# Kernel tuning notes

Measured on AMD Instinct MI355X. Metric: run time of the kernel, lower is better.

## Reference

```python
import math
import jax, jax.numpy as jnp
import numpy as np

B, S, D, H = 4, 2048, 512, 8
DH = D // H
NUM_BUCKETS = 32
MAX_DISTANCE = 128


def _relative_position_bucket(rel_pos, num_buckets=NUM_BUCKETS, max_distance=MAX_DISTANCE):
    # bidirectional T5 bucketing (faithful to the torch staticmethod)
    num_buckets = num_buckets // 2
    rel_buckets = (rel_pos > 0).astype(jnp.int32) * num_buckets
    rel_pos = jnp.abs(rel_pos)
    max_exact = num_buckets // 2
    is_small = rel_pos < max_exact
    # clamp log arg to >=1 element to avoid -inf cast (masked out by is_small anyway)
    rp_f = jnp.maximum(rel_pos, 1).astype(jnp.float32)
    large = max_exact + (
        jnp.log(rp_f / max_exact) / math.log(max_distance / max_exact) * (num_buckets - max_exact)
    ).astype(jnp.int32)
    large = jnp.minimum(large, num_buckets - 1)
    return rel_buckets + jnp.where(is_small, rel_pos, large)


def setup_inputs() -> dict:
    rng = jax.random.key(0)
    ks = jax.random.split(rng, 12)
    s = 0.02
    return {
        'key':   jax.random.normal(ks[0], (B, S, D), jnp.float32),
        'value': jax.random.normal(ks[1], (B, S, D), jnp.float32),
        'query': jax.random.normal(ks[2], (B, S, D), jnp.float32),
        'Wq': jax.random.normal(ks[3], (D, D), jnp.float32) * s,
        'bq': jnp.zeros((D,), jnp.float32),
        'Wk': jax.random.normal(ks[4], (D, D), jnp.float32) * s,
        'bk': jnp.zeros((D,), jnp.float32),
        'Wv': jax.random.normal(ks[5], (D, D), jnp.float32) * s,
        'bv': jnp.zeros((D,), jnp.float32),
        'Wo': jax.random.normal(ks[6], (D, D), jnp.float32) * s,
        'bo': jnp.zeros((D,), jnp.float32),
        'rel_bias': jax.random.normal(ks[7], (NUM_BUCKETS, H), jnp.float32) * s,
        'mask': jax.random.bernoulli(ks[8], 0.5, (B, S, S)),
    }


def reference(key, value, query, Wq, bq, Wk, bk, Wv, bv, Wo, bo, rel_bias, mask):
    def shape(x):  # [B,S,D] -> [B,H,S,DH]
        return x.reshape(B, -1, H, DH).transpose(0, 2, 1, 3)

    q = shape(query @ Wq + bq) / math.sqrt(DH)
    k = shape(key @ Wk + bk)
    v = shape(value @ Wv + bv)

    scores = jnp.einsum('bhqd,bhkd->bhqk', q, k)  # [B,H,S,S]

    # T5 relative position bias
    rel_pos = jnp.arange(S)[None, :] - jnp.arange(S)[:, None]  # [S,S] memory - query
    buckets = _relative_position_bucket(rel_pos)
    pos_bias = rel_bias[buckets]                     # [S,S,H]
    scores = scores + pos_bias.transpose(2, 0, 1)[None]  # [1,H,S,S]

    scores = jnp.where(mask[:, None, :, :], jnp.float32(-1e18), scores)
    attn = jax.nn.softmax(scores, axis=-1)  # dropout p=0 -> identity

    ctx = jnp.einsum('bhqk,bhkd->bhqd', attn, v)
    ctx = ctx.transpose(0, 2, 1, 3).reshape(B, -1, D)
    return ctx @ Wo + bo
```

## Files before the change

### kernel.cpp

```cpp
#include <hip/hip_runtime.h>
#include <hip/hip_bf16.h>
#include <math.h>

#define BB 4
#define SS 2048
#define DD 512
#define HH 8
#define DHH 64
#define KPAD 72
#define GPAD 72
#define LOG2E 1.44269504088896340736f

typedef __attribute__((ext_vector_type(8))) short short8;
typedef __attribute__((ext_vector_type(4))) float f32x4;
typedef __attribute__((ext_vector_type(16))) float f32x16;
typedef __attribute__((ext_vector_type(4))) unsigned short ushort4v;
typedef unsigned short ushort;
typedef unsigned char uchar;
typedef unsigned int u32;
typedef unsigned long long u64;

static __device__ __forceinline__ ushort f2b(float x) {
    __hip_bfloat16 h = __float2bfloat16(x);
    return *reinterpret_cast<ushort*>(&h);
}

__global__ __launch_bounds__(256) void pack_mask_kernel(const void* __restrict__ mask,
                                                        u64* __restrict__ mwords) {
    __shared__ int sflag;
    const int tid = threadIdx.x;
    if (tid == 0) sflag = 0;
    __syncthreads();
    u32 probe = ((const u32*)mask)[tid];
    if (__any(probe > 1u) && (tid & 63) == 0) sflag = 1;
    __syncthreads();
    const bool bytemode = sflag != 0;

    int idx = blockIdx.x * 256 + tid;
    int w = idx & 31;
    int row = idx >> 5;
    u64 bits = 0ull;
    if (bytemode) {
        const uint4* p4 = (const uint4*)((const uchar*)mask + (size_t)row * SS + w * 64);
#pragma unroll
        for (int i = 0; i < 4; ++i) {
            uint4 v = p4[i];
            unsigned int a[4] = {v.x, v.y, v.z, v.w};
#pragma unroll
            for (int j = 0; j < 4; ++j)
#pragma unroll
                for (int byte = 0; byte < 4; ++byte)
                    if ((a[j] >> (byte * 8)) & 0xffu) bits |= 1ull << (i * 16 + j * 4 + byte);
        }
    } else {
        const int4* p4 = (const int4*)((const int*)mask + (size_t)row * SS + w * 64);
#pragma unroll
        for (int i = 0; i < 16; ++i) {
            int4 v = p4[i];
            if (v.x) bits |= 1ull << (i * 4 + 0);
            if (v.y) bits |= 1ull << (i * 4 + 1);
            if (v.z) bits |= 1ull << (i * 4 + 2);
            if (v.w) bits |= 1ull << (i * 4 + 3);
        }
    }
    mwords[idx] = bits;
}

__device__ __forceinline__ int t5_bucket(int rel) {
    int rb = (rel > 0) ? 16 : 0;
    int ap = rel < 0 ? -rel : rel;
    if (ap < 8) return rb + ap;
    float t = logf((float)ap * 0.125f) / 2.77258872985839844f * 8.0f;
    int large = 8 + (int)t;
    if (large > 15) large = 15;
    return rb + large;
}

__global__ __launch_bounds__(256) void bias_table_kernel(const float* __restrict__ rel_bias,
                                                         float* __restrict__ tbl) {
    int i = blockIdx.x * 256 + threadIdx.x;
    int h = i >> 12;
    int d = (i & 4095) - 2047;
    tbl[i] = LOG2E * rel_bias[t5_bucket(d) * HH + h];
}

__global__ __launch_bounds__(256) void wtrans_kernel(const float* __restrict__ W0, const float* __restrict__ W1,
                                                     const float* __restrict__ W2, const float* __restrict__ W3,
                                                     ushort* __restrict__ T0, ushort* __restrict__ T1,
                                                     ushort* __restrict__ T2, ushort* __restrict__ T3) {
    __shared__ float tile[64][65];
    const float* W = blockIdx.z == 0 ? W0 : blockIdx.z == 1 ? W1 : blockIdx.z == 2 ? W2 : W3;
    ushort*     T = blockIdx.z == 0 ? T0 : blockIdx.z == 1 ? T1 : blockIdx.z == 2 ? T2 : T3;
    const int n0 = blockIdx.x * 64, k0 = blockIdx.y * 64;
    const int tr = threadIdx.x >> 4, tc = threadIdx.x & 15;
#pragma unroll
    for (int i = 0; i < 4; ++i) {
        int r = i * 16 + tr;
        float4 v = *(const float4*)&W[(size_t)(k0 + r) * 512 + n0 + tc * 4];
        tile[r][tc * 4 + 0] = v.x; tile[r][tc * 4 + 1] = v.y;
        tile[r][tc * 4 + 2] = v.z; tile[r][tc * 4 + 3] = v.w;
    }
    __syncthreads();
#pragma unroll
    for (int i = 0; i < 4; ++i) {
        int rn = i * 16 + tr;
        ushort4v o;
#pragma unroll
        for (int j = 0; j < 4; ++j) o[j] = f2b(tile[tc * 4 + j][rn]);
        *(ushort4v*)&T[(size_t)(n0 + rn) * 512 + k0 + tc * 4] = o;
    }
}

__global__ __launch_bounds__(256) void qkv_gemm(const float* __restrict__ Xq, const float* __restrict__ Xk,
                                                const float* __restrict__ Xv,
                                                const ushort* __restrict__ Wqt, const ushort* __restrict__ Wkt,
                                                const ushort* __restrict__ Wvt,
                                                const float* __restrict__ bqp, const float* __restrict__ bkp,
                                                const float* __restrict__ bvp,
                                                ushort* __restrict__ Yq, ushort* __restrict__ Yk,
                                                ushort* __restrict__ Yv) {
    __shared__ ushort Als[64 * GPAD];
    __shared__ ushort Bls[128 * GPAD];
    const int z = blockIdx.z;
    const float* A    = z == 0 ? Xq : z == 1 ? Xk : Xv;
    const ushort* Bt  = z == 0 ? Wqt : z == 1 ? Wkt : Wvt;
    const float* bias = z == 0 ? bqp : z == 1 ? bkp : bvp;
    const float scale = z == 0 ? 0.125f * LOG2E : 1.0f;

    const int tid = threadIdx.x;
    const int lane = tid & 63;
    const int wid = tid >> 6;
    const int lq = lane & 15, lg = lane >> 4;
    const int wr = wid >> 1, wc = wid & 1;
    const int bm = blockIdx.x * 64;
    const int bn = blockIdx.y * 128;

    f32x4 acc[2][4];
#pragma unroll
    for (int m = 0; m < 2; ++m)
#pragma unroll
        for (int n = 0; n < 4; ++n) acc[m][n] = (f32x4){0.f, 0.f, 0.f, 0.f};

    for (int k0 = 0; k0 < 512; k0 += 64) {
        __syncthreads();
#pragma unroll
        for (int i = 0; i < 2; ++i) {
            int c = tid + i * 256;
            int r = c >> 3, kc = (c & 7) * 8;
            float4 u = *(const float4*)(A + (size_t)(bm + r) * 512 + k0 + kc);
            float4 v = *(const float4*)(A + (size_t)(bm + r) * 512 + k0 + kc + 4);
            short8 av;
            av[0] = (short)f2b(u.x); av[1] = (short)f2b(u.y); av[2] = (short)f2b(u.z); av[3] = (short)f2b(u.w);
            av[4] = (short)f2b(v.x); av[5] = (short)f2b(v.y); av[6] = (short)f2b(v.z); av[7] = (short)f2b(v.w);
            *(short8*)&Als[r * GPAD + kc] = av;
        }
#pragma unroll
        for (int i = 0; i < 4; ++i) {
            int c = tid + i * 256;
            int r = c >> 3, kc = (c & 7) * 8;
            *(short8*)&Bls[r * GPAD + kc] = *(const short8*)(Bt + (size_t)(bn + r) * 512 + k0 + kc);
        }
        __syncthreads();
#pragma unroll
        for (int kk = 0; kk < 2; ++kk) {
            short8 af[2], bf[4];
#pragma unroll
            for (int m = 0; m < 2; ++m)
                af[m] = *(short8*)&Als[(wr * 32 + m * 16 + lq) * GPAD + kk * 32 + lg * 8];
#pragma unroll
            for (int n = 0; n < 4; ++n)
                bf[n] = *(short8*)&Bls[(wc * 64 + n * 16 + lq) * GPAD + kk * 32 + lg * 8];
#pragma unroll
            for (int m = 0; m < 2; ++m)
#pragma unroll
                for (int n = 0; n < 4; ++n)
                    acc[m][n] = __builtin_amdgcn_mfma_f32_16x16x32_bf16(af[m], bf[n], acc[m][n], 0, 0, 0);
        }
    }

    float bv[4];
#pragma unroll
    for (int n = 0; n < 4; ++n) bv[n] = bias[bn + wc * 64 + n * 16 + lq];

    if (z == 2) {
        const int blk = bm >> 11;
        const int s0 = (bm & 2047) + wr * 32 + lg * 4;
#pragma unroll
        for (int m = 0; m < 2; ++m)
#pragma unroll
            for (int n = 0; n < 4; ++n) {
                int col = bn + wc * 64 + n * 16 + lq;
                ushort4v o;
#pragma unroll
                for (int r = 0; r < 4; ++r) o[r] = f2b(acc[m][n][r] + bv[n]);
                *(ushort4v*)&Yv[((size_t)(blk * 512 + col)) * SS + s0 + m * 16] = o;
            }
    } else {
        ushort* Y = z ? Yk : Yq;
#pragma unroll
        for (int m = 0; m < 2; ++m)
#pragma unroll
            for (int r = 0; r < 4; ++r) {
                int row = bm + wr * 32 + m * 16 + lg * 4 + r;
#pragma unroll
                for (int n = 0; n < 4; ++n) {
                    int col = bn + wc * 64 + n * 16 + lq;
                    Y[(size_t)row * 512 + col] = f2b((acc[m][n][r] + bv[n]) * scale);
                }
            }
    }
}

__global__ __launch_bounds__(256) void out_gemm(const ushort* __restrict__ A,
                                                const ushort* __restrict__ Bt,
                                                const float* __restrict__ bias,
                                                float* __restrict__ Y) {
    __shared__ ushort Als[64 * GPAD];
    __shared__ ushort Bls[128 * GPAD];
    const int tid = threadIdx.x;
    const int lane = tid & 63;
    const int wid = tid >> 6;
    const int lq = lane & 15, lg = lane >> 4;
    const int wr = wid >> 1, wc = wid & 1;
    const int bm = blockIdx.x * 64;
    const int bn = blockIdx.y * 128;

    f32x4 acc[2][4];
#pragma unroll
    for (int m = 0; m < 2; ++m)
#pragma unroll
        for (int n = 0; n < 4; ++n) acc[m][n] = (f32x4){0.f, 0.f, 0.f, 0.f};

    for (int k0 = 0; k0 < 512; k0 += 64) {
        __syncthreads();
#pragma unroll
        for (int i = 0; i < 2; ++i) {
            int c = tid + i * 256;
            int r = c >> 3, kc = (c & 7) * 8;
            *(short8*)&Als[r * GPAD + kc] = *(const short8*)(A + (size_t)(bm + r) * 512 + k0 + kc);
        }
#pragma unroll
        for (int i = 0; i < 4; ++i) {
            int c = tid + i * 256;
            int r = c >> 3, kc = (c & 7) * 8;
            *(short8*)&Bls[r * GPAD + kc] = *(const short8*)(Bt + (size_t)(bn + r) * 512 + k0 + kc);
        }
        __syncthreads();
#pragma unroll
        for (int kk = 0; kk < 2; ++kk) {
            short8 af[2], bf[4];
#pragma unroll
            for (int m = 0; m < 2; ++m)
                af[m] = *(short8*)&Als[(wr * 32 + m * 16 + lq) * GPAD + kk * 32 + lg * 8];
#pragma unroll
            for (int n = 0; n < 4; ++n)
                bf[n] = *(short8*)&Bls[(wc * 64 + n * 16 + lq) * GPAD + kk * 32 + lg * 8];
#pragma unroll
            for (int m = 0; m < 2; ++m)
#pragma unroll
                for (int n = 0; n < 4; ++n)
                    acc[m][n] = __builtin_amdgcn_mfma_f32_16x16x32_bf16(af[m], bf[n], acc[m][n], 0, 0, 0);
        }
    }

    float bv[4];
#pragma unroll
    for (int n = 0; n < 4; ++n) bv[n] = bias[bn + wc * 64 + n * 16 + lq];
#pragma unroll
    for (int m = 0; m < 2; ++m)
#pragma unroll
        for (int r = 0; r < 4; ++r) {
            int row = bm + wr * 32 + m * 16 + lg * 4 + r;
#pragma unroll
            for (int n = 0; n < 4; ++n) {
                int col = bn + wc * 64 + n * 16 + lq;
                Y[(size_t)row * 512 + col] = acc[m][n][r] + bv[n];
            }
        }
}

__global__ __launch_bounds__(512, 4) void attn_kernel(const ushort* __restrict__ Qg, const ushort* __restrict__ Kg,
                                                      const ushort* __restrict__ vT, const u64* __restrict__ mwords,
                                                      const float* __restrict__ btbl, ushort* __restrict__ ctxb) {
    __shared__ ushort KV[4][64 * KPAD];
    __shared__ ushort QT[128 * KPAD];
    float* tbl = (float*)QT;

    const int bid = blockIdx.x;
    const int wk = ((bid & 7) << 6) | (bid >> 3);
    const int qb = wk & 15;
    const int h  = (wk >> 4) & 7;
    const int b  = wk >> 7;
    const int q0 = qb * 128;

    const int tid  = threadIdx.x;
    const int wid  = tid >> 6;
    const int lane = tid & 63;
    const int lq32 = lane & 31;
    const int hi   = lane >> 5;
    const int seg  = wid >> 2;
    const int qw   = wid & 3;

    const u64* mrow = mwords + (size_t)b * SS * 32;
    const int qg = q0 + qw * 32 + lq32;

    {
        const int r = tid >> 2;
        const int c = (tid & 3) * 16;
        const size_t g = ((size_t)(b * SS + q0 + r)) * DD + h * DHH + c;
        *(short8*)&QT[r * KPAD + c]     = *(const short8*)(Qg + g);
        *(short8*)&QT[r * KPAD + c + 8] = *(const short8*)(Qg + g + 8);
    }
    __syncthreads();

    short8 qf[4];
#pragma unroll
    for (int dch = 0; dch < 4; ++dch)
        qf[dch] = *(short8*)&QT[(qw * 32 + lq32) * KPAD + dch * 16 + hi * 8];
    __syncthreads();

    {
        const float4* src = (const float4*)(btbl + (size_t)h * 4096);
        float4* dst = (float4*)tbl;
        dst[tid]       = src[tid];
        dst[tid + 512] = src[tid + 512];
    }

    f32x16 acc0, acc1, accl;
#pragma unroll
    for (int i = 0; i < 16; ++i) { acc0[i] = 0.f; acc1[i] = 0.f; accl[i] = 0.f; }

    short8 ones;
#pragma unroll
    for (int i = 0; i < 8; ++i) ones[i] = (short)0x3F80;

    const int stile = tid >> 7;
    const int sidx = tid & 127;
    const int srow = sidx >> 1;
    const int scol = (sidx & 1) * 32;
    const size_t kbaseK = ((size_t)(b * SS + (stile & 1) * 1024 + srow)) * DD + h * DHH + scol;
    const size_t kbaseV = ((size_t)(b * DD + h * DHH + srow)) * SS + (stile & 1) * 1024 + scol;

    short8 stg[4];
    {
        const ushort* sp = (stile < 2) ? (Kg + kbaseK) : (vT + kbaseV);
#pragma unroll
        for (int j = 0; j < 4; ++j) stg[j] = *(const short8*)(sp + j * 8);
    }

    const float* tbp_base = tbl + (2047 + hi * 4 - qg);

    for (int t = 0; t < 16; ++t) {
        __syncthreads();
        {
            ushort* dst = &KV[stile][srow * KPAD + scol];
#pragma unroll
            for (int j = 0; j < 4; ++j) *(short8*)(dst + j * 8) = stg[j];
        }
        __syncthreads();
        if (t < 15) {
            const ushort* sp = (stile < 2) ? (Kg + kbaseK + (size_t)(t + 1) * 64 * DD)
                                           : (vT + kbaseV + (t + 1) * 64);
#pragma unroll
            for (int j = 0; j < 4; ++j) stg[j] = *(const short8*)(sp + j * 8);
        }

        const ushort* Ks = KV[seg];
        const ushort* Vt = KV[2 + seg];
        const int ktw = seg * 16 + t;
        const u64 wv = mrow[(size_t)qg * 32 + ktw];

        const float* tbp = tbp_base + ktw * 64;
        f32x16 st0, st1;
#pragma unroll
        for (int r = 0; r < 16; ++r) {
            const int br = (r & 3) + 8 * (r >> 2);
            st0[r] = tbp[br];
            st1[r] = tbp[32 + br];
        }
#pragma unroll
        for (int dch = 0; dch < 4; ++dch) {
            short8 kf0 = *(short8*)&Ks[lq32 * KPAD + dch * 16 + hi * 8];
            short8 kf1 = *(short8*)&Ks[(32 + lq32) * KPAD + dch * 16 + hi * 8];
            st0 = __builtin_amdgcn_mfma_f32_32x32x16_bf16(kf0, qf[dch], st0, 0, 0, 0);
            st1 = __builtin_amdgcn_mfma_f32_32x32x16_bf16(kf1, qf[dch], st1, 0, 0, 0);
        }

        const u32 mi0 = ~(((u32)wv) >> (hi * 4));
        const u32 mi1 = ~(((u32)(wv >> 32)) >> (hi * 4));
        float p0[16], p1[16];
#pragma unroll
        for (int r = 0; r < 16; ++r) {
            const int br = (r & 3) + 8 * (r >> 2);
            float e0 = __builtin_amdgcn_exp2f(st0[r]);
            float e1 = __builtin_amdgcn_exp2f(st1[r]);
            u32 k0 = (u32)(((int)(mi0 << (31 - br))) >> 31);
            u32 k1 = (u32)(((int)(mi1 << (31 - br))) >> 31);
            p0[r] = __uint_as_float(__float_as_uint(e0) & k0);
            p1[r] = __uint_as_float(__float_as_uint(e1) & k1);
        }

        u32 W[16];
#pragma unroll
        for (int w = 0; w < 8; ++w) {
            asm("v_cvt_pk_bf16_f32 %0, %1, %2" : "=v"(W[w])     : "v"(p0[2 * w]), "v"(p0[2 * w + 1]));
            asm("v_cvt_pk_bf16_f32 %0, %1, %2" : "=v"(W[8 + w]) : "v"(p1[2 * w]), "v"(p1[2 * w + 1]));
        }
        short8 pf[4];
#pragma unroll
        for (int g = 0; g < 4; ++g) {
            u32 A = W[g * 4 + 0], Bw = W[g * 4 + 1], C = W[g * 4 + 2], D = W[g * 4 + 3];
            asm("v_permlane32_swap_b32 %0, %1" : "+v"(A), "+v"(C));
            asm("v_permlane32_swap_b32 %0, %1" : "+v"(Bw), "+v"(D));
            u32 fr[4] = {A, Bw, C, D};
            pf[g] = *(short8*)fr;
        }

#pragma unroll
        for (int g = 0; g < 4; ++g) {
            short8 vf0 = *(short8*)&Vt[lq32 * KPAD + g * 16 + hi * 8];
            short8 vf1 = *(short8*)&Vt[(32 + lq32) * KPAD + g * 16 + hi * 8];
            acc0 = __builtin_amdgcn_mfma_f32_32x32x16_bf16(vf0, pf[g], acc0, 0, 0, 0);
            acc1 = __builtin_amdgcn_mfma_f32_32x32x16_bf16(vf1, pf[g], acc1, 0, 0, 0);
            accl = __builtin_amdgcn_mfma_f32_32x32x16_bf16(ones, pf[g], accl, 0, 0, 0);
        }
    }

    float l_run = accl[0];

    __syncthreads();
    float* cmb = (float*)KV;
    float* cl  = cmb + 128 * 65;
    const int q = qw * 32 + lq32;
    if (seg == 1) {
#pragma unroll
        for (int r = 0; r < 16; ++r) {
            const int dr = (r & 3) + 8 * (r >> 2) + 4 * hi;
            cmb[q * 65 + dr]      = acc0[r];
            cmb[q * 65 + 32 + dr] = acc1[r];
        }
        if (hi == 0) cl[q] = l_run;
    }
    __syncthreads();
    if (seg == 0) {
#pragma unroll
        for (int r = 0; r < 16; ++r) {
            const int dr = (r & 3) + 8 * (r >> 2) + 4 * hi;
            acc0[r] += cmb[q * 65 + dr];
            acc1[r] += cmb[q * 65 + 32 + dr];
        }
        l_run += cl[q];
        const float linv = 1.0f / l_run;
        ushort* T = QT;
#pragma unroll
        for (int r = 0; r < 16; ++r) {
            const int dr = (r & 3) + 8 * (r >> 2) + 4 * hi;
            T[q * KPAD + dr]      = f2b(acc0[r] * linv);
            T[q * KPAD + 32 + dr] = f2b(acc1[r] * linv);
        }
        const int r2 = qw * 32 + (lane >> 1);
        const int c0 = (lane & 1) * 32;
        const size_t g = ((size_t)(b * SS + q0 + r2)) * DD + h * DHH + c0;
#pragma unroll
        for (int j = 0; j < 4; ++j)
            *(short8*)(ctxb + g + j * 8) = *(short8*)&QT[r2 * KPAD + c0 + j * 8];
    }
}

extern "C" void kernel_launch(void* const* d_in, const int* in_sizes, int n_in,
                              void* d_out, int out_size, void* d_ws, size_t ws_size,
                              hipStream_t stream) {
    const float* key   = (const float*)d_in[0];
    const float* value = (const float*)d_in[1];
    const float* query = (const float*)d_in[2];
    const float* Wq = (const float*)d_in[3];
    const float* bq = (const float*)d_in[4];
    const float* Wk = (const float*)d_in[5];
    const float* bk = (const float*)d_in[6];
    const float* Wv = (const float*)d_in[7];
    const float* bv = (const float*)d_in[8];
    const float* Wo = (const float*)d_in[9];
    const float* bo = (const float*)d_in[10];
    const float* rel_bias = (const float*)d_in[11];
    const void* mask = d_in[12];
    float* out = (float*)d_out;

    char* ws = (char*)d_ws;
    const size_t MB = 1024 * 1024;
    float* btbl   = (float*)(ws + 4096);
    u64* mwords   = (u64*)(ws + 512 * 1024);
    ushort* wq_t  = (ushort*)(ws + (size_t)(3 * MB));
    ushort* wk_t  = wq_t + 512 * 512;
    ushort* wv_t  = wk_t + 512 * 512;
    ushort* wo_t  = wv_t + 512 * 512;
    ushort* q_bf  = (ushort*)(ws + (size_t)(5 * MB));
    ushort* k_bf  = q_bf + (size_t)8192 * 512;
    ushort* vT    = k_bf + (size_t)8192 * 512;
    ushort* ctx_bf = vT + (size_t)8192 * 512;

    hipLaunchKernelGGL(pack_mask_kernel, dim3(BB * SS * 32 / 256), dim3(256), 0, stream,
                       mask, mwords);
    hipLaunchKernelGGL(bias_table_kernel, dim3(HH * 4096 / 256), dim3(256), 0, stream,
                       rel_bias, btbl);
    hipLaunchKernelGGL(wtrans_kernel, dim3(8, 8, 4), dim3(256), 0, stream,
                       Wq, Wk, Wv, Wo, wq_t, wk_t, wv_t, wo_t);

    hipLaunchKernelGGL(qkv_gemm, dim3(128, 4, 3), dim3(256), 0, stream,
                       query, key, value, wq_t, wk_t, wv_t, bq, bk, bv, q_bf, k_bf, vT);

    hipLaunchKernelGGL(attn_kernel, dim3(512), dim3(512), 0, stream,
                       q_bf, k_bf, vT, mwords, btbl, ctx_bf);

    hipLaunchKernelGGL(out_gemm, dim3(128, 4), dim3(256), 0, stream, ctx_bf, wo_t, bo, out);
}
```

Baseline: 128.8 us.

## Merge prep kernels and register-prefetch GEMMs with larger 128x128 tiles

Fuses the mask packing, bias table and weight transpose kernels into a single prep launch to cut launch overhead. Both projection GEMMs now use 512-thread blocks with 128x128 tiles. They prefetch the next K-slice into registers while MFMAs run on the current LDS tile, so global loads overlap compute. The price is more registers per thread, double the LDS for A, and half as many blocks in the grid, which may lower occupancy.

```diff
diff --git a/kernel.cpp b/kernel.cpp
--- a/kernel.cpp
+++ b/kernel.cpp
@@ -25,47 +25,6 @@
     return *reinterpret_cast<ushort*>(&h);
 }
 
-__global__ __launch_bounds__(256) void pack_mask_kernel(const void* __restrict__ mask,
-                                                        u64* __restrict__ mwords) {
-    __shared__ int sflag;
-    const int tid = threadIdx.x;
-    if (tid == 0) sflag = 0;
-    __syncthreads();
-    u32 probe = ((const u32*)mask)[tid];
-    if (__any(probe > 1u) && (tid & 63) == 0) sflag = 1;
-    __syncthreads();
-    const bool bytemode = sflag != 0;
-
-    int idx = blockIdx.x * 256 + tid;
-    int w = idx & 31;
-    int row = idx >> 5;
-    u64 bits = 0ull;
-    if (bytemode) {
-        const uint4* p4 = (const uint4*)((const uchar*)mask + (size_t)row * SS + w * 64);
-#pragma unroll
-        for (int i = 0; i < 4; ++i) {
-            uint4 v = p4[i];
-            unsigned int a[4] = {v.x, v.y, v.z, v.w};
-#pragma unroll
-            for (int j = 0; j < 4; ++j)
-#pragma unroll
-                for (int byte = 0; byte < 4; ++byte)
-                    if ((a[j] >> (byte * 8)) & 0xffu) bits |= 1ull << (i * 16 + j * 4 + byte);
-        }
-    } else {
-        const int4* p4 = (const int4*)((const int*)mask + (size_t)row * SS + w * 64);
-#pragma unroll
-        for (int i = 0; i < 16; ++i) {
-            int4 v = p4[i];
-            if (v.x) bits |= 1ull << (i * 4 + 0);
-            if (v.y) bits |= 1ull << (i * 4 + 1);
-            if (v.z) bits |= 1ull << (i * 4 + 2);
-            if (v.w) bits |= 1ull << (i * 4 + 3);
-        }
-    }
-    mwords[idx] = bits;
-}
-
 __device__ __forceinline__ int t5_bucket(int rel) {
     int rb = (rel > 0) ? 16 : 0;
     int ap = rel < 0 ? -rel : rel;
@@ -76,42 +35,85 @@
     return rb + large;
 }
 
-__global__ __launch_bounds__(256) void bias_table_kernel(const float* __restrict__ rel_bias,
-                                                         float* __restrict__ tbl) {
-    int i = blockIdx.x * 256 + threadIdx.x;
-    int h = i >> 12;
-    int d = (i & 4095) - 2047;
-    tbl[i] = LOG2E * rel_bias[t5_bucket(d) * HH + h];
-}
-
-__global__ __launch_bounds__(256) void wtrans_kernel(const float* __restrict__ W0, const float* __restrict__ W1,
-                                                     const float* __restrict__ W2, const float* __restrict__ W3,
-                                                     ushort* __restrict__ T0, ushort* __restrict__ T1,
-                                                     ushort* __restrict__ T2, ushort* __restrict__ T3) {
+__global__ __launch_bounds__(256) void prep_kernel(const void* __restrict__ mask, u64* __restrict__ mwords,
+                                                   const float* __restrict__ rel_bias, float* __restrict__ btbl,
+                                                   const float* __restrict__ W0, const float* __restrict__ W1,
+                                                   const float* __restrict__ W2, const float* __restrict__ W3,
+                                                   ushort* __restrict__ T0, ushort* __restrict__ T1,
+                                                   ushort* __restrict__ T2, ushort* __restrict__ T3) {
     __shared__ float tile[64][65];
-    const float* W = blockIdx.z == 0 ? W0 : blockIdx.z == 1 ? W1 : blockIdx.z == 2 ? W2 : W3;
-    ushort*     T = blockIdx.z == 0 ? T0 : blockIdx.z == 1 ? T1 : blockIdx.z == 2 ? T2 : T3;
-    const int n0 = blockIdx.x * 64, k0 = blockIdx.y * 64;
-    const int tr = threadIdx.x >> 4, tc = threadIdx.x & 15;
-#pragma unroll
-    for (int i = 0; i < 4; ++i) {
-        int r = i * 16 + tr;
-        float4 v = *(const float4*)&W[(size_t)(k0 + r) * 512 + n0 + tc * 4];
-        tile[r][tc * 4 + 0] = v.x; tile[r][tc * 4 + 1] = v.y;
-        tile[r][tc * 4 + 2] = v.z; tile[r][tc * 4 + 3] = v.w;
-    }
-    __syncthreads();
-#pragma unroll
-    for (int i = 0; i < 4; ++i) {
-        int rn = i * 16 + tr;
-        ushort4v o;
-#pragma unroll
-        for (int j = 0; j < 4; ++j) o[j] = f2b(tile[tc * 4 + j][rn]);
-        *(ushort4v*)&T[(size_t)(n0 + rn) * 512 + k0 + tc * 4] = o;
-    }
-}
-
-__global__ __launch_bounds__(256) void qkv_gemm(const float* __restrict__ Xq, const float* __restrict__ Xk,
+    __shared__ int sflag;
+    const int bid = blockIdx.x;
+    const int tid = threadIdx.x;
+
+    if (bid < 1024) {
+        if (tid == 0) sflag = 0;
+        __syncthreads();
+        u32 probe = ((const u32*)mask)[tid];
+        if (__any(probe > 1u) && (tid & 63) == 0) sflag = 1;
+        __syncthreads();
+        const bool bytemode = sflag != 0;
+
+        int idx = bid * 256 + tid;
+        int w = idx & 31;
+        int row = idx >> 5;
+        u64 bits = 0ull;
+        if (bytemode) {
+            const uint4* p4 = (const uint4*)((const uchar*)mask + (size_t)row * SS + w * 64);
+#pragma unroll
+            for (int i = 0; i < 4; ++i) {
+                uint4 v = p4[i];
+                unsigned int a[4] = {v.x, v.y, v.z, v.w};
+#pragma unroll
+                for (int j = 0; j < 4; ++j)
+#pragma unroll
+                    for (int byte = 0; byte < 4; ++byte)
+                        if ((a[j] >> (byte * 8)) & 0xffu) bits |= 1ull << (i * 16 + j * 4 + byte);
+            }
+        } else {
+            const int4* p4 = (const int4*)((const int*)mask + (size_t)row * SS + w * 64);
+#pragma unroll
+            for (int i = 0; i < 16; ++i) {
+                int4 v = p4[i];
+                if (v.x) bits |= 1ull << (i * 4 + 0);
+                if (v.y) bits |= 1ull << (i * 4 + 1);
+                if (v.z) bits |= 1ull << (i * 4 + 2);
+                if (v.w) bits |= 1ull << (i * 4 + 3);
+            }
+        }
+        mwords[idx] = bits;
+    } else if (bid < 1152) {
+        int i = (bid - 1024) * 256 + tid;
+        int h = i >> 12;
+        int d = (i & 4095) - 2047;
+        btbl[i] = LOG2E * rel_bias[t5_bucket(d) * HH + h];
+    } else {
+        const int b2 = bid - 1152;
+        const int z = b2 >> 6;
+        const float* W = z == 0 ? W0 : z == 1 ? W1 : z == 2 ? W2 : W3;
+        ushort*     T = z == 0 ? T0 : z == 1 ? T1 : z == 2 ? T2 : T3;
+        const int n0 = (b2 & 7) * 64, k0 = ((b2 >> 3) & 7) * 64;
+        const int tr = tid >> 4, tc = tid & 15;
+#pragma unroll
+        for (int i = 0; i < 4; ++i) {
+            int r = i * 16 + tr;
+            float4 v = *(const float4*)&W[(size_t)(k0 + r) * 512 + n0 + tc * 4];
+            tile[r][tc * 4 + 0] = v.x; tile[r][tc * 4 + 1] = v.y;
+            tile[r][tc * 4 + 2] = v.z; tile[r][tc * 4 + 3] = v.w;
+        }
+        __syncthreads();
+#pragma unroll
+        for (int i = 0; i < 4; ++i) {
+            int rn = i * 16 + tr;
+            ushort4v o;
+#pragma unroll
+            for (int j = 0; j < 4; ++j) o[j] = f2b(tile[tc * 4 + j][rn]);
+            *(ushort4v*)&T[(size_t)(n0 + rn) * 512 + k0 + tc * 4] = o;
+        }
+    }
+}
+
+__global__ __launch_bounds__(512) void qkv_gemm(const float* __restrict__ Xq, const float* __restrict__ Xk,
                                                 const float* __restrict__ Xv,
                                                 const ushort* __restrict__ Wqt, const ushort* __restrict__ Wkt,
                                                 const ushort* __restrict__ Wvt,
@@ -119,7 +121,7 @@
                                                 const float* __restrict__ bvp,
                                                 ushort* __restrict__ Yq, ushort* __restrict__ Yk,
                                                 ushort* __restrict__ Yv) {
-    __shared__ ushort Als[64 * GPAD];
+    __shared__ ushort Als[128 * GPAD];
     __shared__ ushort Bls[128 * GPAD];
     const int z = blockIdx.z;
     const float* A    = z == 0 ? Xq : z == 1 ? Xk : Xv;
@@ -132,7 +134,7 @@
     const int wid = tid >> 6;
     const int lq = lane & 15, lg = lane >> 4;
     const int wr = wid >> 1, wc = wid & 1;
-    const int bm = blockIdx.x * 64;
+    const int bm = blockIdx.x * 128;
     const int bn = blockIdx.y * 128;
 
     f32x4 acc[2][4];
@@ -141,26 +143,43 @@
 #pragma unroll
         for (int n = 0; n < 4; ++n) acc[m][n] = (f32x4){0.f, 0.f, 0.f, 0.f};
 
+    short8 sa[2], sb[2];
+#pragma unroll
+    for (int i = 0; i < 2; ++i) {
+        int c = tid + i * 512;
+        int r = c >> 3, kc = (c & 7) * 8;
+        float4 u = *(const float4*)(A + (size_t)(bm + r) * 512 + kc);
+        float4 v = *(const float4*)(A + (size_t)(bm + r) * 512 + kc + 4);
+        short8 av;
+        av[0] = (short)f2b(u.x); av[1] = (short)f2b(u.y); av[2] = (short)f2b(u.z); av[3] = (short)f2b(u.w);
+        av[4] = (short)f2b(v.x); av[5] = (short)f2b(v.y); av[6] = (short)f2b(v.z); av[7] = (short)f2b(v.w);
+        sa[i] = av;
+        sb[i] = *(const short8*)(Bt + (size_t)(bn + r) * 512 + kc);
+    }
+
     for (int k0 = 0; k0 < 512; k0 += 64) {
-        __syncthreads();
 #pragma unroll
         for (int i = 0; i < 2; ++i) {
-            int c = tid + i * 256;
+            int c = tid + i * 512;
             int r = c >> 3, kc = (c & 7) * 8;
-            float4 u = *(const float4*)(A + (size_t)(bm + r) * 512 + k0 + kc);
-            float4 v = *(const float4*)(A + (size_t)(bm + r) * 512 + k0 + kc + 4);
-            short8 av;
-            av[0] = (short)f2b(u.x); av[1] = (short)f2b(u.y); av[2] = (short)f2b(u.z); av[3] = (short)f2b(u.w);
-            av[4] = (short)f2b(v.x); av[5] = (short)f2b(v.y); av[6] = (short)f2b(v.z); av[7] = (short)f2b(v.w);
-            *(short8*)&Als[r * GPAD + kc] = av;
-        }
-#pragma unroll
-        for (int i = 0; i < 4; ++i) {
-            int c = tid + i * 256;
-            int r = c >> 3, kc = (c & 7) * 8;
-            *(short8*)&Bls[r * GPAD + kc] = *(const short8*)(Bt + (size_t)(bn + r) * 512 + k0 + kc);
-        }
-        __syncthreads();
+            *(short8*)&Als[r * GPAD + kc] = sa[i];
+            *(short8*)&Bls[r * GPAD + kc] = sb[i];
+        }
+        __syncthreads();
+        if (k0 < 448) {
+#pragma unroll
+            for (int i = 0; i < 2; ++i) {
+                int c = tid + i * 512;
+                int r = c >> 3, kc = (c & 7) * 8;
+                float4 u = *(const float4*)(A + (size_t)(bm + r) * 512 + k0 + 64 + kc);
+                float4 v = *(const float4*)(A + (size_t)(bm + r) * 512 + k0 + 64 + kc + 4);
+                short8 av;
+                av[0] = (short)f2b(u.x); av[1] = (short)f2b(u.y); av[2] = (short)f2b(u.z); av[3] = (short)f2b(u.w);
+                av[4] = (short)f2b(v.x); av[5] = (short)f2b(v.y); av[6] = (short)f2b(v.z); av[7] = (short)f2b(v.w);
+                sa[i] = av;
+                sb[i] = *(const short8*)(Bt + (size_t)(bn + r) * 512 + k0 + 64 + kc);
+            }
+        }
 #pragma unroll
         for (int kk = 0; kk < 2; ++kk) {
             short8 af[2], bf[4];
@@ -176,6 +195,7 @@
                 for (int n = 0; n < 4; ++n)
                     acc[m][n] = __builtin_amdgcn_mfma_f32_16x16x32_bf16(af[m], bf[n], acc[m][n], 0, 0, 0);
         }
+        __syncthreads();
     }
 
     float bv[4];
@@ -211,18 +231,18 @@
     }
 }
 
-__global__ __launch_bounds__(256) void out_gemm(const ushort* __restrict__ A,
+__global__ __launch_bounds__(512) void out_gemm(const ushort* __restrict__ A,
                                                 const ushort* __restrict__ Bt,
                                                 const float* __restrict__ bias,
                                                 float* __restrict__ Y) {
-    __shared__ ushort Als[64 * GPAD];
+    __shared__ ushort Als[128 * GPAD];
     __shared__ ushort Bls[128 * GPAD];
     const int tid = threadIdx.x;
     const int lane = tid & 63;
     const int wid = tid >> 6;
     const int lq = lane & 15, lg = lane >> 4;
     const int wr = wid >> 1, wc = wid & 1;
-    const int bm = blockIdx.x * 64;
+    const int bm = blockIdx.x * 128;
     const int bn = blockIdx.y * 128;
 
     f32x4 acc[2][4];
@@ -231,21 +251,33 @@
 #pragma unroll
         for (int n = 0; n < 4; ++n) acc[m][n] = (f32x4){0.f, 0.f, 0.f, 0.f};
 
+    short8 sa[2], sb[2];
+#pragma unroll
+    for (int i = 0; i < 2; ++i) {
+        int c = tid + i * 512;
+        int r = c >> 3, kc = (c & 7) * 8;
+        sa[i] = *(const short8*)(A + (size_t)(bm + r) * 512 + kc);
+        sb[i] = *(const short8*)(Bt + (size_t)(bn + r) * 512 + kc);
+    }
+
     for (int k0 = 0; k0 < 512; k0 += 64) {
-        __syncthreads();
 #pragma unroll
         for (int i = 0; i < 2; ++i) {
-            int c = tid + i * 256;
+            int c = tid + i * 512;
             int r = c >> 3, kc = (c & 7) * 8;
-            *(short8*)&Als[r * GPAD + kc] = *(const short8*)(A + (size_t)(bm + r) * 512 + k0 + kc);
-        }
-#pragma unroll
-        for (int i = 0; i < 4; ++i) {
-            int c = tid + i * 256;
-            int r = c >> 3, kc = (c & 7) * 8;
-            *(short8*)&Bls[r * GPAD + kc] = *(const short8*)(Bt + (size_t)(bn + r) * 512 + k0 + kc);
-        }
-        __syncthreads();
+            *(short8*)&Als[r * GPAD + kc] = sa[i];
+            *(short8*)&Bls[r * GPAD + kc] = sb[i];
+        }
+        __syncthreads();
+        if (k0 < 448) {
+#pragma unroll
+            for (int i = 0; i < 2; ++i) {
+                int c = tid + i * 512;
+                int r = c >> 3, kc = (c & 7) * 8;
+                sa[i] = *(const short8*)(A + (size_t)(bm + r) * 512 + k0 + 64 + kc);
+                sb[i] = *(const short8*)(Bt + (size_t)(bn + r) * 512 + k0 + 64 + kc);
+            }
+        }
 #pragma unroll
         for (int kk = 0; kk < 2; ++kk) {
             short8 af[2], bf[4];
@@ -261,6 +293,7 @@
                 for (int n = 0; n < 4; ++n)
                     acc[m][n] = __builtin_amdgcn_mfma_f32_16x16x32_bf16(af[m], bf[n], acc[m][n], 0, 0, 0);
         }
+        __syncthreads();
     }
 
     float bv[4];
@@ -498,18 +531,15 @@
     ushort* vT    = k_bf + (size_t)8192 * 512;
     ushort* ctx_bf = vT + (size_t)8192 * 512;
 
-    hipLaunchKernelGGL(pack_mask_kernel, dim3(BB * SS * 32 / 256), dim3(256), 0, stream,
-                       mask, mwords);
-    hipLaunchKernelGGL(bias_table_kernel, dim3(HH * 4096 / 256), dim3(256), 0, stream,
-                       rel_bias, btbl);
-    hipLaunchKernelGGL(wtrans_kernel, dim3(8, 8, 4), dim3(256), 0, stream,
+    hipLaunchKernelGGL(prep_kernel, dim3(1408), dim3(256), 0, stream,
+                       mask, mwords, rel_bias, btbl,
                        Wq, Wk, Wv, Wo, wq_t, wk_t, wv_t, wo_t);
 
-    hipLaunchKernelGGL(qkv_gemm, dim3(128, 4, 3), dim3(256), 0, stream,
+    hipLaunchKernelGGL(qkv_gemm, dim3(64, 4, 3), dim3(512), 0, stream,
                        query, key, value, wq_t, wk_t, wv_t, bq, bk, bv, q_bf, k_bf, vT);
 
     hipLaunchKernelGGL(attn_kernel, dim3(512), dim3(512), 0, stream,
                        q_bf, k_bf, vT, mwords, btbl, ctx_bf);
 
-    hipLaunchKernelGGL(out_gemm, dim3(128, 4), dim3(256), 0, stream, ctx_bf, wo_t, bo, out);
-}
+    hipLaunchKernelGGL(out_gemm, dim3(64, 4), dim3(512), 0, stream, ctx_bf, wo_t, bo, out);
+}
```

Result: faster. 111.3 us (-13.5%).
